# Kernel optimization log

Hardware: AMD Instinct MI355X
Metric: run time of the kernel (lower is better)

## Reference

```python
import jax, jax.numpy as jnp
import numpy as np

B, L, C, H, W = 8, 8, 64, 56, 56
K = 3
EPS = 1e-5


def setup_inputs() -> dict:
    key = jax.random.key(0)
    ks = jax.random.split(key, 7)
    s = lambda k, shape, sc=0.05: jax.random.normal(k, shape, dtype=jnp.float32) * sc
    return {
        "x": jax.random.normal(ks[0], (B, L, C, H, W), dtype=jnp.float32),
        "temporal_w": s(ks[1], (C, C)),        # Conv3d 1x1x1 C->C
        "temporal_b": s(ks[2], (C,)),
        "fc_w": s(ks[3], (C,)),                # Conv3d 1x1x1 C->1
        "fc_b": s(ks[4], (1,)),
        "conv_w": s(ks[5], (C, C, K, K), 0.1), # self.weight [1,1,Co,Ci,k,k] core
        "conv_b": s(ks[6], (C,)),              # self.bias [1,1,Co] core
        "bn_gamma": jnp.ones((C,), jnp.float32),
        "bn_beta": jnp.zeros((C,), jnp.float32),
    }


def reference(x, temporal_w, temporal_b, fc_w, fc_b, conv_w, conv_b, bn_gamma, bn_beta):
    b, l, c, h, w = x.shape
    # ---- generateweight_fourier ----
    xin = jnp.transpose(x, (0, 2, 1, 3, 4))                # [B,C,L,H,W]
    f = jnp.fft.fft2(xin, axes=(3, 4), norm='ortho')       # spatial FFT
    f = jnp.fft.fft(f, axis=2, norm='ortho')               # temporal FFT
    allxin = xin + 0.01 * jnp.abs(f) * xin                 # Fourier2 attention + residual
    pooled = allxin.mean(axis=(3, 4))                      # AdaptiveAvgPool3d((None,1,1)) -> [B,C,L]
    # temporalconv: 1x1x1 Conv3d C->C on [B,C,L,1,1]
    calib = jnp.einsum('oc,bcl->bol', temporal_w, pooled) + temporal_b[None, :, None]  # [B,C,L]
    # fc: 1x1x1 Conv3d C->1
    fcout = jnp.einsum('c,bcl->bl', fc_w, pooled) + fc_b[0]                            # [B,L]
    # finalweight: weight[1,1,Co,Ci,k,k] * (calib+1) broadcast over Ci -> [B,L,Co,Ci,k,k]
    calib_blc = jnp.transpose(calib, (0, 2, 1)) + 1.0      # [B,L,Ci]
    fw = conv_w[None, None] * calib_blc[:, :, None, :, None, None]
    fb = conv_b[None, None, :] * (fcout + 1.0)[:, :, None] # [B,L,Co]
    # ---- dynamic per-(sample,frame) conv2d (groups = b*l) ----
    x_flat = x.reshape(b * l, c, h, w)
    fw_flat = fw.reshape(b * l, c, c, K, K)
    fb_flat = fb.reshape(b * l, c)

    def per_sample(xi, wi):
        return jax.lax.conv_general_dilated(
            xi[None], wi, window_strides=(1, 1), padding=[(1, 1), (1, 1)],
            dimension_numbers=('NCHW', 'OIHW', 'NCHW'))[0]

    out = jax.vmap(per_sample)(x_flat, fw_flat) + fb_flat[:, :, None, None]
    out = x_flat + out                                     # residual (gate=False)
    # BatchNorm2d (training-mode batch statistics)
    mean = out.mean(axis=(0, 2, 3), keepdims=True)
    var = out.var(axis=(0, 2, 3), keepdims=True)
    out = (out - mean) * jax.lax.rsqrt(var + EPS)
    out = out * bn_gamma[None, :, None, None] + bn_beta[None, :, None, None]
    out = out * jax.nn.sigmoid(out)                        # SiLU
    return out.reshape(b, l, c, h, w)
```

## Files before the change

kernel.cpp:

```cpp
#include <hip/hip_runtime.h>
#include <cmath>

#define HW 3136
#define NF 64
#define NBLK2 448

typedef __attribute__((ext_vector_type(8))) short short8;
typedef __attribute__((ext_vector_type(4))) float float4a;

__device__ __forceinline__ unsigned short f2bf(float f) {
    unsigned int u = __float_as_uint(f);
    u += 0x7fffu + ((u >> 16) & 1u);
    return (unsigned short)(u >> 16);
}
__device__ __forceinline__ float bf2f(unsigned short u) {
    return __uint_as_float(((unsigned int)u) << 16);
}

__global__ __launch_bounds__(256)
void pack_kernel(const float* __restrict__ cw,
                 unsigned short* __restrict__ Ffix,
                 unsigned short* __restrict__ Wp) {
    if (blockIdx.x < 64) {
        int idx = blockIdx.x * 256 + threadIdx.x;
        int j    = idx & 7;
        int lane = (idx >> 3) & 63;
        int ks   = (idx >> 9) & 3;
        int t    = (idx >> 11) & 3;
        int p    = (idx >> 13) & 1;
        int mn = t * 16 + (lane & 15);
        int k  = ks * 32 + (lane >> 4) * 8 + j;
        float val = 0.f;
        if (mn < 56 && k < 112) {
            int kk = (k < 56) ? k : k - 56;
            int prod = (mn * kk) % 56;
            float ang = -6.2831853071795864f * (float)prod / 56.0f;
            float cr = cosf(ang);
            float ci = sinf(ang);
            float first  = (p == 0) ? cr : ci;
            float second = (p == 0) ? -ci : cr;
            val = (k < 56) ? first : second;
        }
        Ffix[idx] = f2bf(val);
    } else {
        int idx = (blockIdx.x - 64) * 256 + threadIdx.x;
        if (idx < 36864) {
            int i  = idx & 63;
            int o  = (idx >> 6) & 63;
            int kk = idx >> 12;
            Wp[idx] = f2bf(cw[(o * 64 + i) * 9 + kk]);
        }
    }
}

__global__ __launch_bounds__(256, 2)
void fft_mfma_kernel(const float* __restrict__ x,
                     const unsigned short* __restrict__ Ffix,
                     float* __restrict__ pooled) {
    const int bc = blockIdx.x;
    const int c  = bc & 63;
    const int b  = bc >> 6;
    const int tid  = threadIdx.x;
    const int lane = tid & 63;
    const int wv   = tid >> 6;
    const int n    = lane & 15;
    const int q    = lane >> 4;

    __shared__ unsigned short sh[40352];
    unsigned short* xbf = sh;
    unsigned short* Tb  = sh + 25088;
    unsigned short* Ub  = sh + 25088 + 56 * 136;
    float* red = (float*)(sh + 40320);

    for (int t = tid; t < 7616; t += 256)
        ((unsigned int*)(sh + 25088))[t] = 0u;

    for (int t = tid; t < 6272; t += 256) {
        int l = t / 784, r = t - l * 784;
        float4 v = *(const float4*)(x + ((size_t)((b * 8 + l) * 64 + c)) * HW + r * 4);
        ushort4 o;
        o.x = f2bf(v.x); o.y = f2bf(v.y); o.z = f2bf(v.z); o.w = f2bf(v.w);
        *(ushort4*)(xbf + l * 3136 + r * 4) = o;
    }
    __syncthreads();

    #pragma unroll 1
    for (int lp = 0; lp < 5; ++lp) {
        float tr[8], ti[8];
        #pragma unroll
        for (int l = 0; l < 8; ++l) {
            float ang = -0.78539816339744831f * (float)((l * lp) & 7);
            tr[l] = cosf(ang);
            ti[l] = sinf(ang);
        }
        for (int s = tid; s < 784; s += 256) {
            int h = s / 14, w4 = s - h * 14;
            float re[4] = {0.f, 0.f, 0.f, 0.f}, im[4] = {0.f, 0.f, 0.f, 0.f};
            #pragma unroll
            for (int l = 0; l < 8; ++l) {
                ushort4 u = *(const ushort4*)(xbf + l * 3136 + h * 56 + w4 * 4);
                float v0 = bf2f(u.x), v1 = bf2f(u.y), v2 = bf2f(u.z), v3 = bf2f(u.w);
                re[0] += v0 * tr[l]; im[0] += v0 * ti[l];
                re[1] += v1 * tr[l]; im[1] += v1 * ti[l];
                re[2] += v2 * tr[l]; im[2] += v2 * ti[l];
                re[3] += v3 * tr[l]; im[3] += v3 * ti[l];
            }
            #pragma unroll
            for (int j = 0; j < 4; ++j) {
                int w = w4 * 4 + j;
                Tb[w * 136 + h]      = f2bf(re[j]);
                Tb[w * 136 + 56 + h] = f2bf(im[j]);
            }
        }
        __syncthreads();

        {
            const int p  = wv >> 1;
            const int mh = (wv & 1) * 2;
            float4a s1[2][4];
            #pragma unroll
            for (int mi = 0; mi < 2; ++mi)
                #pragma unroll
                for (int nt = 0; nt < 4; ++nt) s1[mi][nt] = (float4a){0.f, 0.f, 0.f, 0.f};
            #pragma unroll
            for (int ks = 0; ks < 4; ++ks) {
                short8 bfr[4];
                #pragma unroll
                for (int nt = 0; nt < 4; ++nt) {
                    int row = nt * 16 + n; if (row > 55) row = 55;
                    bfr[nt] = *(const short8*)(Tb + row * 136 + ks * 32 + q * 8);
                }
                #pragma unroll
                for (int mi = 0; mi < 2; ++mi) {
                    short8 afr = *(const short8*)(Ffix + ((((p * 4 + mh + mi) * 4 + ks) * 64 + lane) * 8));
                    #pragma unroll
                    for (int nt = 0; nt < 4; ++nt)
                        s1[mi][nt] = __builtin_amdgcn_mfma_f32_16x16x32_bf16(afr, bfr[nt], s1[mi][nt], 0, 0, 0);
                }
            }
            #pragma unroll
            for (int mi = 0; mi < 2; ++mi)
                #pragma unroll
                for (int nt = 0; nt < 4; ++nt)
                    #pragma unroll
                    for (int r = 0; r < 4; ++r) {
                        int kh = (mh + mi) * 16 + q * 4 + r;
                        int w  = nt * 16 + n;
                        if (kh < 56 && w < 56)
                            Ub[kh * 136 + p * 56 + w] = f2bf(s1[mi][nt][r]);
                    }
        }
        __syncthreads();

        const int mt = wv;
        short8 afr2[4];
        #pragma unroll
        for (int ks = 0; ks < 4; ++ks) {
            int row = mt * 16 + n; if (row > 55) row = 55;
            afr2[ks] = *(const short8*)(Ub + row * 136 + ks * 32 + q * 8);
        }
        float4a g[2][4];
        #pragma unroll
        for (int pp = 0; pp < 2; ++pp)
            #pragma unroll
            for (int nt = 0; nt < 4; ++nt) g[pp][nt] = (float4a){0.f, 0.f, 0.f, 0.f};
        #pragma unroll
        for (int pp = 0; pp < 2; ++pp)
            #pragma unroll
            for (int ks = 0; ks < 4; ++ks)
                #pragma unroll
                for (int nt = 0; nt < 4; ++nt) {
                    short8 bfr = *(const short8*)(Ffix + ((((pp * 4 + nt) * 4 + ks) * 64 + lane) * 8));
                    g[pp][nt] = __builtin_amdgcn_mfma_f32_16x16x32_bf16(afr2[ks], bfr, g[pp][nt], 0, 0, 0);
                }

        const bool doflip = (lp >= 1 && lp <= 3);
        const unsigned short* x1 = xbf + lp * 3136;
        const unsigned short* x2 = xbf + ((8 - lp) & 7) * 3136;
        float S1 = 0.f, X1 = 0.f, S2 = 0.f, X2 = 0.f;
        #pragma unroll
        for (int nt = 0; nt < 4; ++nt) {
            int kw = nt * 16 + n;
            if (kw < 56) {
                int kwf = (56 - kw) % 56;
                #pragma unroll
                for (int r = 0; r < 4; ++r) {
                    int kh = mt * 16 + q * 4 + r;
                    if (kh < 56) {
                        float gr = g[0][nt][r], gi = g[1][nt][r];
                        float mag = sqrtf(gr * gr + gi * gi);
                        float v1 = bf2f(x1[kh * 56 + kw]);
                        S1 += mag * v1; X1 += v1;
                        if (doflip) {
                            int khf = (56 - kh) % 56;
                            float v2 = bf2f(x2[khf * 56 + kwf]);
                            S2 += mag * v2; X2 += v2;
                        }
                    }
                }
            }
        }
        #pragma unroll
        for (int m = 1; m < 64; m <<= 1) {
            S1 += __shfl_xor(S1, m);
            X1 += __shfl_xor(X1, m);
            S2 += __shfl_xor(S2, m);
            X2 += __shfl_xor(X2, m);
        }
        if (lane == 0) { red[wv * 4 + 0] = S1; red[wv * 4 + 1] = X1;
                         red[wv * 4 + 2] = S2; red[wv * 4 + 3] = X2; }
        __syncthreads();
        if (tid == 0) {
            float s1 = 0.f, xs1 = 0.f, s2 = 0.f, xs2 = 0.f;
            #pragma unroll
            for (int w = 0; w < 4; ++w) {
                s1 += red[w * 4 + 0]; xs1 += red[w * 4 + 1];
                s2 += red[w * 4 + 2]; xs2 += red[w * 4 + 3];
            }
            const float kS = 0.01f / (56.0f * 2.8284271247461903f);
            pooled[bc * 8 + lp] = (xs1 + kS * s1) / 3136.0f;
            if (doflip)
                pooled[bc * 8 + (8 - lp)] = (xs2 + kS * s2) / 3136.0f;
        }
    }
}

__global__ __launch_bounds__(64)
void calib_kernel(const float* __restrict__ pooled,
                  const float* __restrict__ tw_, const float* __restrict__ tb,
                  const float* __restrict__ fcw, const float* __restrict__ fcb,
                  const float* __restrict__ convb,
                  float* __restrict__ scale, float* __restrict__ fbias) {
    const int nn = blockIdx.x;
    const int b = nn >> 3, l = nn & 7;
    const int o = threadIdx.x;
    const float* pr = pooled + b * 512 + l;
    float dot = 0.f;
    #pragma unroll 8
    for (int c0 = 0; c0 < 64; ++c0) dot += tw_[o * 64 + c0] * pr[c0 * 8];
    float fcp = fcw[o] * pr[o * 8];
    #pragma unroll
    for (int off = 32; off > 0; off >>= 1) fcp += __shfl_down(fcp, off);
    float fcout = __shfl(fcp, 0) + fcb[0];
    scale[nn * 64 + o] = 1.0f + tb[o] + dot;
    fbias[nn * 64 + o] = convb[o] * (fcout + 1.0f);
}

__global__ __launch_bounds__(256, 2)
void conv_mfma_kernel(const float* __restrict__ x,
                      const unsigned short* __restrict__ Wp,
                      const float* __restrict__ scale, const float* __restrict__ fbias,
                      float* __restrict__ out,
                      float* __restrict__ psum, float* __restrict__ psum2) {
    const int rt = blockIdx.x;
    const int nn = blockIdx.y;
    const int tid  = threadIdx.x;
    const int lane = tid & 63;
    const int wv   = tid >> 6;
    const int r0   = rt * 8;

    __shared__ unsigned short xs[10 * 60 * 64];
    __shared__ float fb[64], ssc[64], rsc[64], bn1[64], bn2[64];

    if (tid < 64) {
        fb[tid]  = fbias[nn * 64 + tid];
        float s  = scale[nn * 64 + tid];
        ssc[tid] = s;
        rsc[tid] = 1.0f / s;
        bn1[tid] = 0.f; bn2[tid] = 0.f;
    }
    __syncthreads();

    for (int t = tid; t < 10240; t += 256) {
        if (t < 8960) {
            int c4 = t % 14;
            int rr = (t / 14) % 10;
            int i  = t / 140;
            int gr = r0 - 1 + rr;
            float4 v = make_float4(0.f, 0.f, 0.f, 0.f);
            if (gr >= 0 && gr < 56)
                v = *(const float4*)(x + ((size_t)(nn * 64 + i) * HW + gr * 56 + c4 * 4));
            float s = ssc[i];
            int g = i >> 3, il = i & 7;
            float vv[4] = {v.x, v.y, v.z, v.w};
            #pragma unroll
            for (int j = 0; j < 4; ++j) {
                int lc = c4 * 4 + 1 + j;
                xs[(rr * 60 + lc) * 64 + (((g ^ (lc & 7)) << 3) | il)] = f2bf(vv[j] * s);
            }
        } else {
            int idx = t - 8960;
            int i   = idx / 20;
            int rem = idx - i * 20;
            int rr  = rem >> 1;
            int lc  = (rem & 1) * 57;
            int g = i >> 3, il = i & 7;
            xs[(rr * 60 + lc) * 64 + (((g ^ (lc & 7)) << 3) | il)] = 0;
        }
    }
    __syncthreads();

    const int pxo = lane & 15;
    const int q   = lane >> 4;

    float4a acc[7][4];
    #pragma unroll
    for (int j = 0; j < 7; ++j)
        #pragma unroll
        for (int ot = 0; ot < 4; ++ot) acc[j][ot] = (float4a){0.f, 0.f, 0.f, 0.f};

    int rp[7], cp[7];
    #pragma unroll
    for (int j = 0; j < 7; ++j) {
        int px = (wv * 7 + j) * 16 + pxo;
        rp[j] = px / 56;
        cp[j] = px - rp[j] * 56;
    }

    #pragma unroll 1
    for (int kk = 0; kk < 9; ++kk) {
        const int dr = kk / 3, dc = kk - dr * 3;
        short8 a[4][2];
        #pragma unroll
        for (int ot = 0; ot < 4; ++ot)
            #pragma unroll
            for (int ih = 0; ih < 2; ++ih)
                a[ot][ih] = *(const short8*)(Wp + ((kk * 64 + ot * 16 + pxo) * 64 + ih * 32 + q * 8));

        #pragma unroll
        for (int j = 0; j < 7; ++j) {
            int lc = cp[j] + dc;
            int base = ((rp[j] + dr) * 60 + lc) * 64;
            int sw = lc & 7;
            #pragma unroll
            for (int ih = 0; ih < 2; ++ih) {
                short8 bv = *(const short8*)&xs[base + (((q + ih * 4) ^ sw) << 3)];
                #pragma unroll
                for (int ot = 0; ot < 4; ++ot)
                    acc[j][ot] = __builtin_amdgcn_mfma_f32_16x16x32_bf16(a[ot][ih], bv, acc[j][ot], 0, 0, 0);
            }
        }
    }

    float bs[4][4], bs2[4][4];
    #pragma unroll
    for (int ot = 0; ot < 4; ++ot)
        #pragma unroll
        for (int r = 0; r < 4; ++r) { bs[ot][r] = 0.f; bs2[ot][r] = 0.f; }

    #pragma unroll
    for (int j = 0; j < 7; ++j) {
        int px  = (wv * 7 + j) * 16 + pxo;
        int gpx = r0 * 56 + px;
        int rr  = rp[j] + 1;
        int lc  = cp[j] + 1;
        int sw  = lc & 7;
        int rowbase = (rr * 60 + lc) * 64;
        #pragma unroll
        for (int ot = 0; ot < 4; ++ot) {
            int g  = ot * 2 + (q >> 1);
            ushort4 uu = *(const ushort4*)(xs + rowbase + (((g ^ sw) << 3) | ((q & 1) * 4)));
            float resid[4] = {bf2f(uu.x), bf2f(uu.y), bf2f(uu.z), bf2f(uu.w)};
            #pragma unroll
            for (int r = 0; r < 4; ++r) {
                int o = ot * 16 + q * 4 + r;
                size_t off = (size_t)(nn * 64 + o) * HW + gpx;
                float v = acc[j][ot][r] + resid[r] * rsc[o] + fb[o];
                out[off] = v;
                bs[ot][r]  += v;
                bs2[ot][r] += v * v;
            }
        }
    }
    #pragma unroll
    for (int ot = 0; ot < 4; ++ot)
        #pragma unroll
        for (int r = 0; r < 4; ++r) {
            #pragma unroll
            for (int m = 1; m < 16; m <<= 1) {
                bs[ot][r]  += __shfl_xor(bs[ot][r], m);
                bs2[ot][r] += __shfl_xor(bs2[ot][r], m);
            }
        }
    if (pxo == 0) {
        #pragma unroll
        for (int ot = 0; ot < 4; ++ot)
            #pragma unroll
            for (int r = 0; r < 4; ++r) {
                int o = ot * 16 + q * 4 + r;
                atomicAdd(&bn1[o], bs[ot][r]);
                atomicAdd(&bn2[o], bs2[ot][r]);
            }
    }
    __syncthreads();
    if (tid < 64) {
        int bl = nn * 7 + rt;
        psum[bl * 64 + tid]  = bn1[tid];
        psum2[bl * 64 + tid] = bn2[tid];
    }
}

__global__ __launch_bounds__(256)
void bnstat_kernel(const float* __restrict__ psum, const float* __restrict__ psum2,
                   float* __restrict__ bn) {
    const int o = blockIdx.x;
    const int tid = threadIdx.x;
    float s = 0.f, s2 = 0.f;
    for (int bl = tid; bl < NBLK2; bl += 256) {
        s  += psum[bl * 64 + o];
        s2 += psum2[bl * 64 + o];
    }
    __shared__ float r1[256], r2[256];
    r1[tid] = s; r2[tid] = s2;
    __syncthreads();
    for (int st = 128; st > 0; st >>= 1) {
        if (tid < st) { r1[tid] += r1[tid + st]; r2[tid] += r2[tid + st]; }
        __syncthreads();
    }
    if (tid == 0) {
        const float N = 64.0f * (float)HW;
        float mean = r1[0] / N;
        float var  = r2[0] / N - mean * mean;
        bn[o]      = mean;
        bn[64 + o] = rsqrtf(var + 1e-5f);
    }
}

__global__ __launch_bounds__(256)
void bnsilu_kernel(float* __restrict__ out, const float* __restrict__ bn,
                   const float* __restrict__ gamma, const float* __restrict__ beta) {
    size_t idx = (size_t)blockIdx.x * 256 + threadIdx.x;
    if (idx >= (size_t)NF * 64 * HW) return;
    int c = (int)((idx / HW) & 63);
    float v = out[idx];
    float y = (v - bn[c]) * bn[64 + c] * gamma[c] + beta[c];
    out[idx] = y / (1.0f + expf(-y));
}

extern "C" void kernel_launch(void* const* d_in, const int* in_sizes, int n_in,
                              void* d_out, int out_size, void* d_ws, size_t ws_size,
                              hipStream_t stream) {
    const float* x          = (const float*)d_in[0];
    const float* temporal_w = (const float*)d_in[1];
    const float* temporal_b = (const float*)d_in[2];
    const float* fc_w       = (const float*)d_in[3];
    const float* fc_b       = (const float*)d_in[4];
    const float* conv_w     = (const float*)d_in[5];
    const float* conv_b     = (const float*)d_in[6];
    const float* bn_gamma   = (const float*)d_in[7];
    const float* bn_beta    = (const float*)d_in[8];
    float* out = (float*)d_out;
    float* ws  = (float*)d_ws;

    float* pooled = ws;
    float* scale  = ws + 4096;
    float* fbias  = ws + 8192;
    unsigned short* Wp = (unsigned short*)(ws + 12288);
    float* psum   = ws + 12288 + 18432;
    float* psum2  = psum + NBLK2 * 64;
    float* bn     = psum2 + NBLK2 * 64;
    unsigned short* Ffix = (unsigned short*)(bn + 128);

    pack_kernel<<<208, 256, 0, stream>>>(conv_w, Ffix, Wp);
    fft_mfma_kernel<<<512, 256, 0, stream>>>(x, Ffix, pooled);
    calib_kernel<<<64, 64, 0, stream>>>(pooled, temporal_w, temporal_b,
                                        fc_w, fc_b, conv_b, scale, fbias);
    conv_mfma_kernel<<<dim3(7, 64), 256, 0, stream>>>(x, Wp, scale, fbias,
                                                      out, psum, psum2);
    bnstat_kernel<<<64, 256, 0, stream>>>(psum, psum2, bn);
    int total = NF * 64 * HW;
    bnsilu_kernel<<<(total + 255) / 256, 256, 0, stream>>>(out, bn, bn_gamma, bn_beta);
}
```

Before: 224.4 us.

## Use 512 threads in FFT kernel with per-wave tiles and staged magnitude reduction

The Fourier pooling kernel doubles its block to 8 waves, so each wave computes a single 16-row tile of each DFT matmul stage instead of two. The second-stage complex result is staged through shared memory (reusing the transpose buffers) so the magnitude-weighted sum runs as a flat strided loop over all threads. Per-frame plain sums are computed once up front instead of once per frequency pass, and only the padding columns are zeroed each pass. This adds extra barriers and an LDS round trip for the result, and the launch bound of 4 blocks of 512 threads may constrain registers and LDS occupancy.

```diff
diff --git a/kernel.cpp b/kernel.cpp
--- a/kernel.cpp
+++ b/kernel.cpp
@@ -53,7 +53,7 @@
     }
 }
 
-__global__ __launch_bounds__(256, 2)
+__global__ __launch_bounds__(512, 4)
 void fft_mfma_kernel(const float* __restrict__ x,
                      const unsigned short* __restrict__ Ffix,
                      float* __restrict__ pooled) {
@@ -66,16 +66,15 @@
     const int n    = lane & 15;
     const int q    = lane >> 4;
 
-    __shared__ unsigned short sh[40352];
+    __shared__ unsigned short sh[40320];
     unsigned short* xbf = sh;
     unsigned short* Tb  = sh + 25088;
     unsigned short* Ub  = sh + 25088 + 56 * 136;
-    float* red = (float*)(sh + 40320);
-
-    for (int t = tid; t < 7616; t += 256)
-        ((unsigned int*)(sh + 25088))[t] = 0u;
-
-    for (int t = tid; t < 6272; t += 256) {
+    float* G = (float*)(sh + 25088);
+    __shared__ float xsum[8];
+    __shared__ float red[16];
+
+    for (int t = tid; t < 6272; t += 512) {
         int l = t / 784, r = t - l * 784;
         float4 v = *(const float4*)(x + ((size_t)((b * 8 + l) * 64 + c)) * HW + r * 4);
         ushort4 o;
@@ -84,8 +83,21 @@
     }
     __syncthreads();
 
+    {
+        float s = 0.f;
+        for (int i = lane; i < 3136; i += 64) s += bf2f(xbf[wv * 3136 + i]);
+        #pragma unroll
+        for (int m = 1; m < 64; m <<= 1) s += __shfl_xor(s, m);
+        if (lane == 0) xsum[wv] = s;
+    }
+
     #pragma unroll 1
     for (int lp = 0; lp < 5; ++lp) {
+        for (int t = tid; t < 1344; t += 512) {
+            int row = t / 12;
+            ((unsigned int*)(sh + 25088))[row * 68 + 56 + (t - row * 12)] = 0u;
+        }
+
         float tr[8], ti[8];
         #pragma unroll
         for (int l = 0; l < 8; ++l) {
@@ -93,7 +105,7 @@
             tr[l] = cosf(ang);
             ti[l] = sinf(ang);
         }
-        for (int s = tid; s < 784; s += 256) {
+        for (int s = tid; s < 784; s += 512) {
             int h = s / 14, w4 = s - h * 14;
             float re[4] = {0.f, 0.f, 0.f, 0.f}, im[4] = {0.f, 0.f, 0.f, 0.f};
             #pragma unroll
@@ -115,113 +127,99 @@
         __syncthreads();
 
         {
-            const int p  = wv >> 1;
-            const int mh = (wv & 1) * 2;
-            float4a s1[2][4];
-            #pragma unroll
-            for (int mi = 0; mi < 2; ++mi)
-                #pragma unroll
-                for (int nt = 0; nt < 4; ++nt) s1[mi][nt] = (float4a){0.f, 0.f, 0.f, 0.f};
+            const int p  = wv >> 2;
+            const int mt = wv & 3;
+            float4a s1[4];
+            #pragma unroll
+            for (int nt = 0; nt < 4; ++nt) s1[nt] = (float4a){0.f, 0.f, 0.f, 0.f};
             #pragma unroll
             for (int ks = 0; ks < 4; ++ks) {
-                short8 bfr[4];
+                short8 afr = *(const short8*)(Ffix + ((((p * 4 + mt) * 4 + ks) * 64 + lane) * 8));
                 #pragma unroll
                 for (int nt = 0; nt < 4; ++nt) {
                     int row = nt * 16 + n; if (row > 55) row = 55;
-                    bfr[nt] = *(const short8*)(Tb + row * 136 + ks * 32 + q * 8);
+                    short8 bfr = *(const short8*)(Tb + row * 136 + ks * 32 + q * 8);
+                    s1[nt] = __builtin_amdgcn_mfma_f32_16x16x32_bf16(afr, bfr, s1[nt], 0, 0, 0);
                 }
+            }
+            #pragma unroll
+            for (int nt = 0; nt < 4; ++nt)
                 #pragma unroll
-                for (int mi = 0; mi < 2; ++mi) {
-                    short8 afr = *(const short8*)(Ffix + ((((p * 4 + mh + mi) * 4 + ks) * 64 + lane) * 8));
-                    #pragma unroll
-                    for (int nt = 0; nt < 4; ++nt)
-                        s1[mi][nt] = __builtin_amdgcn_mfma_f32_16x16x32_bf16(afr, bfr[nt], s1[mi][nt], 0, 0, 0);
+                for (int r = 0; r < 4; ++r) {
+                    int kh = mt * 16 + q * 4 + r;
+                    int w  = nt * 16 + n;
+                    if (kh < 56 && w < 56)
+                        Ub[kh * 136 + p * 56 + w] = f2bf(s1[nt][r]);
                 }
-            }
-            #pragma unroll
-            for (int mi = 0; mi < 2; ++mi)
-                #pragma unroll
-                for (int nt = 0; nt < 4; ++nt)
-                    #pragma unroll
-                    for (int r = 0; r < 4; ++r) {
-                        int kh = (mh + mi) * 16 + q * 4 + r;
-                        int w  = nt * 16 + n;
-                        if (kh < 56 && w < 56)
-                            Ub[kh * 136 + p * 56 + w] = f2bf(s1[mi][nt][r]);
-                    }
-        }
-        __syncthreads();
-
-        const int mt = wv;
+        }
+        __syncthreads();
+
+        const int mt = wv & 3;
+        const int pp = wv >> 2;
         short8 afr2[4];
         #pragma unroll
         for (int ks = 0; ks < 4; ++ks) {
             int row = mt * 16 + n; if (row > 55) row = 55;
             afr2[ks] = *(const short8*)(Ub + row * 136 + ks * 32 + q * 8);
         }
-        float4a g[2][4];
-        #pragma unroll
-        for (int pp = 0; pp < 2; ++pp)
-            #pragma unroll
-            for (int nt = 0; nt < 4; ++nt) g[pp][nt] = (float4a){0.f, 0.f, 0.f, 0.f};
-        #pragma unroll
-        for (int pp = 0; pp < 2; ++pp)
-            #pragma unroll
-            for (int ks = 0; ks < 4; ++ks)
-                #pragma unroll
-                for (int nt = 0; nt < 4; ++nt) {
-                    short8 bfr = *(const short8*)(Ffix + ((((pp * 4 + nt) * 4 + ks) * 64 + lane) * 8));
-                    g[pp][nt] = __builtin_amdgcn_mfma_f32_16x16x32_bf16(afr2[ks], bfr, g[pp][nt], 0, 0, 0);
-                }
+        float4a g[4];
+        #pragma unroll
+        for (int nt = 0; nt < 4; ++nt) g[nt] = (float4a){0.f, 0.f, 0.f, 0.f};
+        #pragma unroll
+        for (int ks = 0; ks < 4; ++ks)
+            #pragma unroll
+            for (int nt = 0; nt < 4; ++nt) {
+                short8 bfr = *(const short8*)(Ffix + ((((pp * 4 + nt) * 4 + ks) * 64 + lane) * 8));
+                g[nt] = __builtin_amdgcn_mfma_f32_16x16x32_bf16(afr2[ks], bfr, g[nt], 0, 0, 0);
+            }
+        __syncthreads();
+
+        #pragma unroll
+        for (int nt = 0; nt < 4; ++nt) {
+            int kw = nt * 16 + n;
+            #pragma unroll
+            for (int r = 0; r < 4; ++r) {
+                int kh = mt * 16 + q * 4 + r;
+                if (kh < 56 && kw < 56)
+                    G[pp * 3192 + kh * 57 + kw] = g[nt][r];
+            }
+        }
+        __syncthreads();
 
         const bool doflip = (lp >= 1 && lp <= 3);
         const unsigned short* x1 = xbf + lp * 3136;
         const unsigned short* x2 = xbf + ((8 - lp) & 7) * 3136;
-        float S1 = 0.f, X1 = 0.f, S2 = 0.f, X2 = 0.f;
-        #pragma unroll
-        for (int nt = 0; nt < 4; ++nt) {
-            int kw = nt * 16 + n;
-            if (kw < 56) {
-                int kwf = (56 - kw) % 56;
-                #pragma unroll
-                for (int r = 0; r < 4; ++r) {
-                    int kh = mt * 16 + q * 4 + r;
-                    if (kh < 56) {
-                        float gr = g[0][nt][r], gi = g[1][nt][r];
-                        float mag = sqrtf(gr * gr + gi * gi);
-                        float v1 = bf2f(x1[kh * 56 + kw]);
-                        S1 += mag * v1; X1 += v1;
-                        if (doflip) {
-                            int khf = (56 - kh) % 56;
-                            float v2 = bf2f(x2[khf * 56 + kwf]);
-                            S2 += mag * v2; X2 += v2;
-                        }
-                    }
-                }
+        float S1 = 0.f, S2 = 0.f;
+        for (int t = tid; t < 3136; t += 512) {
+            int kh = t / 56;
+            int kw = t - kh * 56;
+            float gr = G[kh * 57 + kw];
+            float gi = G[3192 + kh * 57 + kw];
+            float mag = sqrtf(gr * gr + gi * gi);
+            S1 += mag * bf2f(x1[t]);
+            if (doflip) {
+                int khf = kh ? 56 - kh : 0;
+                int kwf = kw ? 56 - kw : 0;
+                S2 += mag * bf2f(x2[khf * 56 + kwf]);
             }
         }
         #pragma unroll
         for (int m = 1; m < 64; m <<= 1) {
             S1 += __shfl_xor(S1, m);
-            X1 += __shfl_xor(X1, m);
             S2 += __shfl_xor(S2, m);
-            X2 += __shfl_xor(X2, m);
-        }
-        if (lane == 0) { red[wv * 4 + 0] = S1; red[wv * 4 + 1] = X1;
-                         red[wv * 4 + 2] = S2; red[wv * 4 + 3] = X2; }
+        }
+        if (lane == 0) { red[wv * 2] = S1; red[wv * 2 + 1] = S2; }
         __syncthreads();
         if (tid == 0) {
-            float s1 = 0.f, xs1 = 0.f, s2 = 0.f, xs2 = 0.f;
-            #pragma unroll
-            for (int w = 0; w < 4; ++w) {
-                s1 += red[w * 4 + 0]; xs1 += red[w * 4 + 1];
-                s2 += red[w * 4 + 2]; xs2 += red[w * 4 + 3];
-            }
+            float s1 = 0.f, s2 = 0.f;
+            #pragma unroll
+            for (int w = 0; w < 8; ++w) { s1 += red[w * 2]; s2 += red[w * 2 + 1]; }
             const float kS = 0.01f / (56.0f * 2.8284271247461903f);
-            pooled[bc * 8 + lp] = (xs1 + kS * s1) / 3136.0f;
+            pooled[bc * 8 + lp] = (xsum[lp] + kS * s1) / 3136.0f;
             if (doflip)
-                pooled[bc * 8 + (8 - lp)] = (xs2 + kS * s2) / 3136.0f;
-        }
+                pooled[bc * 8 + (8 - lp)] = (xsum[8 - lp] + kS * s2) / 3136.0f;
+        }
+        __syncthreads();
     }
 }
 
@@ -462,7 +460,7 @@
     unsigned short* Ffix = (unsigned short*)(bn + 128);
 
     pack_kernel<<<208, 256, 0, stream>>>(conv_w, Ffix, Wp);
-    fft_mfma_kernel<<<512, 256, 0, stream>>>(x, Ffix, pooled);
+    fft_mfma_kernel<<<512, 512, 0, stream>>>(x, Ffix, pooled);
     calib_kernel<<<64, 64, 0, stream>>>(pooled, temporal_w, temporal_b,
                                         fc_w, fc_b, conv_b, scale, fbias);
     conv_mfma_kernel<<<dim3(7, 64), 256, 0, stream>>>(x, Wp, scale, fbias,
```

Result: slower. 236.9 us (+5.6%).

## Interleave re/im in FFT LDS buffers and precompute per-frame x sums

Applied to the files above, without the earlier changes.

The intermediate LDS buffers Tb and Ub now store real and imaginary parts interleaved, and the DFT matrix packing is reordered to match. Stores are packed into 32-bit writes with a rotated index to spread LDS bank accesses. Per-frame sums of x are computed once up front instead of being accumulated and reduced in every lp iteration, which drops two of the four shuffle reductions per pass. This risks mismatches if the Ffix k-ordering does not line up with the B-fragment reads in the line that is not shown.

```diff
diff --git a/kernel.cpp b/kernel.cpp
--- a/kernel.cpp
+++ b/kernel.cpp
@@ -32,14 +32,13 @@
         int k  = ks * 32 + (lane >> 4) * 8 + j;
         float val = 0.f;
         if (mn < 56 && k < 112) {
-            int kk = (k < 56) ? k : k - 56;
-            int prod = (mn * kk) % 56;
+            int h = k >> 1;
+            int prod = (mn * h) % 56;
             float ang = -6.2831853071795864f * (float)prod / 56.0f;
             float cr = cosf(ang);
             float ci = sinf(ang);
-            float first  = (p == 0) ? cr : ci;
-            float second = (p == 0) ? -ci : cr;
-            val = (k < 56) ? first : second;
+            if (p == 0) val = (k & 1) ? -ci : cr;
+            else        val = (k & 1) ?  cr : ci;
         }
         Ffix[idx] = f2bf(val);
     } else {
@@ -66,11 +65,12 @@
     const int n    = lane & 15;
     const int q    = lane >> 4;
 
-    __shared__ unsigned short sh[40352];
+    __shared__ unsigned short sh[40320];
     unsigned short* xbf = sh;
     unsigned short* Tb  = sh + 25088;
     unsigned short* Ub  = sh + 25088 + 56 * 136;
-    float* red = (float*)(sh + 40320);
+    __shared__ float xsum[8];
+    __shared__ float red[8];
 
     for (int t = tid; t < 7616; t += 256)
         ((unsigned int*)(sh + 25088))[t] = 0u;
@@ -83,6 +83,20 @@
         *(ushort4*)(xbf + l * 3136 + r * 4) = o;
     }
     __syncthreads();
+
+    {
+        float s0 = 0.f, s4 = 0.f;
+        for (int i = lane; i < 3136; i += 64) {
+            s0 += bf2f(xbf[wv * 3136 + i]);
+            s4 += bf2f(xbf[(wv + 4) * 3136 + i]);
+        }
+        #pragma unroll
+        for (int m = 1; m < 64; m <<= 1) {
+            s0 += __shfl_xor(s0, m);
+            s4 += __shfl_xor(s4, m);
+        }
+        if (lane == 0) { xsum[wv] = s0; xsum[wv + 4] = s4; }
+    }
 
     #pragma unroll 1
     for (int lp = 0; lp < 5; ++lp) {
@@ -106,10 +120,12 @@
                 re[3] += v3 * tr[l]; im[3] += v3 * ti[l];
             }
             #pragma unroll
-            for (int j = 0; j < 4; ++j) {
+            for (int jj = 0; jj < 4; ++jj) {
+                int j = (jj + w4) & 3;
                 int w = w4 * 4 + j;
-                Tb[w * 136 + h]      = f2bf(re[j]);
-                Tb[w * 136 + 56 + h] = f2bf(im[j]);
+                unsigned int pk = (unsigned int)f2bf(re[j])
+                                | ((unsigned int)f2bf(im[j]) << 16);
+                ((unsigned int*)Tb)[w * 68 + h] = pk;
             }
         }
         __syncthreads();
@@ -147,7 +163,7 @@
                         int kh = (mh + mi) * 16 + q * 4 + r;
                         int w  = nt * 16 + n;
                         if (kh < 56 && w < 56)
-                            Ub[kh * 136 + p * 56 + w] = f2bf(s1[mi][nt][r]);
+                            Ub[kh * 136 + 2 * w + p] = f2bf(s1[mi][nt][r]);
                     }
         }
         __syncthreads();
@@ -177,7 +193,7 @@
         const bool doflip = (lp >= 1 && lp <= 3);
         const unsigned short* x1 = xbf + lp * 3136;
         const unsigned short* x2 = xbf + ((8 - lp) & 7) * 3136;
-        float S1 = 0.f, X1 = 0.f, S2 = 0.f, X2 = 0.f;
+        float S1 = 0.f, S2 = 0.f;
         #pragma unroll
         for (int nt = 0; nt < 4; ++nt) {
             int kw = nt * 16 + n;
@@ -189,12 +205,10 @@
                     if (kh < 56) {
                         float gr = g[0][nt][r], gi = g[1][nt][r];
                         float mag = sqrtf(gr * gr + gi * gi);
-                        float v1 = bf2f(x1[kh * 56 + kw]);
-                        S1 += mag * v1; X1 += v1;
+                        S1 += mag * bf2f(x1[kh * 56 + kw]);
                         if (doflip) {
                             int khf = (56 - kh) % 56;
-                            float v2 = bf2f(x2[khf * 56 + kwf]);
-                            S2 += mag * v2; X2 += v2;
+                            S2 += mag * bf2f(x2[khf * 56 + kwf]);
                         }
                     }
                 }
@@ -203,24 +217,18 @@
         #pragma unroll
         for (int m = 1; m < 64; m <<= 1) {
             S1 += __shfl_xor(S1, m);
-            X1 += __shfl_xor(X1, m);
             S2 += __shfl_xor(S2, m);
-            X2 += __shfl_xor(X2, m);
-        }
-        if (lane == 0) { red[wv * 4 + 0] = S1; red[wv * 4 + 1] = X1;
-                         red[wv * 4 + 2] = S2; red[wv * 4 + 3] = X2; }
+        }
+        if (lane == 0) { red[wv * 2] = S1; red[wv * 2 + 1] = S2; }
         __syncthreads();
         if (tid == 0) {
-            float s1 = 0.f, xs1 = 0.f, s2 = 0.f, xs2 = 0.f;
-            #pragma unroll
-            for (int w = 0; w < 4; ++w) {
-                s1 += red[w * 4 + 0]; xs1 += red[w * 4 + 1];
-                s2 += red[w * 4 + 2]; xs2 += red[w * 4 + 3];
-            }
+            float s1 = 0.f, s2 = 0.f;
+            #pragma unroll
+            for (int w = 0; w < 4; ++w) { s1 += red[w * 2]; s2 += red[w * 2 + 1]; }
             const float kS = 0.01f / (56.0f * 2.8284271247461903f);
-            pooled[bc * 8 + lp] = (xs1 + kS * s1) / 3136.0f;
+            pooled[bc * 8 + lp] = (xsum[lp] + kS * s1) / 3136.0f;
             if (doflip)
-                pooled[bc * 8 + (8 - lp)] = (xs2 + kS * s2) / 3136.0f;
+                pooled[bc * 8 + (8 - lp)] = (xsum[8 - lp] + kS * s2) / 3136.0f;
         }
     }
 }
```

New measurement: 232.2 us. +3.5%, slower.
